# Kernel tuning notes

Hardware: AMD Instinct MI355X
Metric: run time of the kernel (lower is better)

## Reference

```python
import jax, jax.numpy as jnp
import numpy as np

NUM_BINS = 256


def setup_inputs() -> dict:
    key = jax.random.key(0)
    k1, k2 = jax.random.split(key)
    shape = (16, 3, 512, 512)
    I_complementary = jax.random.uniform(k1, shape, dtype=jnp.float32)
    I_target = jax.random.uniform(k2, shape, dtype=jnp.float32)
    return {"I_complementary": I_complementary, "I_target": I_target}


def reference(I_complementary, I_target):
    nb = NUM_BINS
    x = I_complementary.reshape(-1)
    y = I_target.reshape(-1)
    bx = jnp.clip(x * (nb - 1), 0, nb - 1).astype(jnp.int32)
    by = jnp.clip(y * (nb - 1), 0, nb - 1).astype(jnp.int32)
    # NOTE: torch's `hist[bx, by] += 1` is index_put WITHOUT accumulation, so
    # duplicate (bx,by) pairs all write old_value+1 = 1: the histogram is a
    # binary occupancy map, not counts. We replicate that with .at[].max(1).
    hist_2d = jnp.zeros((nb, nb), dtype=jnp.float32).at[bx, by].max(1.0)
    hist_2d = hist_2d / hist_2d.sum()
    p_x = hist_2d.sum(axis=1)  # [nb]
    p_y = hist_2d.sum(axis=0)  # [nb]
    mask = hist_2d > 0
    denom = p_x[:, None] * p_y[None, :] + 1e-10
    ratio = jnp.where(mask, hist_2d / denom, 1.0)
    mi = jnp.sum(jnp.where(mask, hist_2d * jnp.log(ratio), 0.0))
    return 1.0 - jnp.tanh(mi)
```

## Files before the change

kernel.cpp:

```cpp
#include <hip/hip_runtime.h>
#include <math.h>


#define NB 256
#define BM_WORDS 2048
#define HGRID 512
#define HTHREADS 512
#define RGRID 64
#define RTHREADS 256

#define SL_WORDS (HGRID * BM_WORDS)

__device__ __forceinline__ void set_bin(unsigned int* bm, float a, float b) {
    float va = fminf(fmaxf(a * 255.0f, 0.0f), 255.0f);
    float vb = fminf(fmaxf(b * 255.0f, 0.0f), 255.0f);
    int bin = ((int)va << 8) | (int)vb;
    atomicOr(&bm[bin >> 5], 1u << (bin & 31));
}

__device__ __forceinline__ void set_bin4(unsigned int* bm, float4 a, float4 b) {
    set_bin(bm, a.x, b.x); set_bin(bm, a.y, b.y);
    set_bin(bm, a.z, b.z); set_bin(bm, a.w, b.w);
}

__device__ __forceinline__ void finalize_from_lds(unsigned int* w, float* rcs, float* red,
                                                  int t, float* out) {
    float partial = 0.0f;
    int r = 0, c = 0;
    if (t < NB) {
#pragma unroll
        for (int k = 0; k < 8; ++k) r += __popc(w[t * 8 + k]);
        rcs[t] = (float)r;
        const int wsel = t >> 5;
        const int bsel = t & 31;
        for (int i = 0; i < NB; ++i) c += (w[i * 8 + wsel] >> bsel) & 1;
    }
    __syncthreads();
    float S = 0.0f;
    if (t < NB) {
        for (int i = 0; i < NB; ++i) S += rcs[i];
        if (r > 0) partial += (float)r * logf((float)r / S);
        if (c > 0) partial += (float)c * logf((float)c / S);
        for (int off = 32; off > 0; off >>= 1) partial += __shfl_down(partial, off, 64);
        if ((t & 63) == 0) red[t >> 6] = partial;
    }
    __syncthreads();
    if (t == 0) {
        float B = red[0] + red[1] + red[2] + red[3];
        float mi = -logf(S) - B / S;
        out[0] = 1.0f - tanhf(mi);
    }
}

__device__ __forceinline__ void hist_body(const float* __restrict__ x,
                                          const float* __restrict__ y,
                                          unsigned int* bm, int n, int t) {
    const int n4 = n >> 2;
    const float4* __restrict__ x4 = (const float4*)x;
    const float4* __restrict__ y4 = (const float4*)y;
    const int nth = gridDim.x * blockDim.x;
    int i = blockIdx.x * blockDim.x + t;

    if (i < n4) {
        float4 a0 = x4[i];
        float4 b0 = y4[i];
        int inext = i + nth;
        while (inext < n4) {
            float4 a1 = x4[inext];
            float4 b1 = y4[inext];
            inext += nth;
            set_bin4(bm, a0, b0);
            a0 = a1; b0 = b1;
        }
        set_bin4(bm, a0, b0);
    }
    for (int j = (n4 << 2) + blockIdx.x * blockDim.x + t; j < n; j += nth) {
        set_bin(bm, x[j], y[j]);
    }
}


__global__ __launch_bounds__(HTHREADS, 2) void hist_slices(const float* __restrict__ x,
                                                           const float* __restrict__ y,
                                                           unsigned int* __restrict__ ws,
                                                           int n) {
    __shared__ unsigned int bm[BM_WORDS];
    const int t = threadIdx.x;
    if (blockIdx.x == 0 && t == 0) ws[SL_WORDS + BM_WORDS] = 0u;
    for (int k = t; k < BM_WORDS; k += HTHREADS) bm[k] = 0u;
    __syncthreads();

    hist_body(x, y, bm, n, t);
    __syncthreads();

    uint4 v;
    v.x = bm[4 * t];     v.y = bm[4 * t + 1];
    v.z = bm[4 * t + 2]; v.w = bm[4 * t + 3];
    ((uint4*)(ws + (size_t)blockIdx.x * BM_WORDS))[t] = v;
}

__global__ __launch_bounds__(RTHREADS) void reduce_finalize(unsigned int* __restrict__ ws,
                                                            float* __restrict__ out) {
    __shared__ uint4 p4[RTHREADS];
    __shared__ unsigned int w[BM_WORDS];
    __shared__ float rcs[NB];
    __shared__ float red[8];
    __shared__ unsigned int ticket;
    const int t = threadIdx.x;
    const int b = blockIdx.x;
    unsigned int* finalbm = ws + SL_WORDS;
    unsigned int* counter = ws + SL_WORDS + BM_WORDS;

    const uint4* s4 = (const uint4*)ws;
    const int q = b * 8 + (t & 7);
    uint4 v = make_uint4(0u, 0u, 0u, 0u);
#pragma unroll 4
    for (int k = 0; k < HGRID / 32; ++k) {
        int s = (t >> 3) + 32 * k;
        uint4 g = s4[(size_t)s * (BM_WORDS / 4) + q];
        v.x |= g.x; v.y |= g.y; v.z |= g.z; v.w |= g.w;
    }
    p4[t] = v;
    __syncthreads();
    if (t < 8) {
        uint4 r = p4[t];
        for (int k = 1; k < 32; ++k) {
            uint4 g = p4[t + 8 * k];
            r.x |= g.x; r.y |= g.y; r.z |= g.z; r.w |= g.w;
        }
        ((uint4*)finalbm)[b * 8 + t] = r;
    }
    __syncthreads();

    if (t == 0) {
        __threadfence();
        ticket = atomicAdd(counter, 1u);
    }
    __syncthreads();
    if (ticket != gridDim.x - 1) return;

    __threadfence();
    for (int k = t; k < BM_WORDS; k += RTHREADS)
        w[k] = __hip_atomic_load(&finalbm[k], __ATOMIC_RELAXED, __HIP_MEMORY_SCOPE_AGENT);
    __syncthreads();
    finalize_from_lds(w, rcs, red, t, out);
}


__global__ void zero_kernel(unsigned int* __restrict__ bm) {
    int i = blockIdx.x * blockDim.x + threadIdx.x;
    if (i < BM_WORDS + 1) bm[i] = 0u;
}

__global__ __launch_bounds__(HTHREADS, 2) void hist_fused(const float* __restrict__ x,
                                                          const float* __restrict__ y,
                                                          unsigned int* __restrict__ gbm,
                                                          float* __restrict__ out,
                                                          int n) {
    __shared__ unsigned int bm[BM_WORDS];
    __shared__ float rcs[NB];
    __shared__ float red[8];
    __shared__ unsigned int ticket;
    const int t = threadIdx.x;

    for (int k = t; k < BM_WORDS; k += blockDim.x) bm[k] = 0u;
    __syncthreads();
    hist_body(x, y, bm, n, t);
    __syncthreads();
    for (int k = t; k < BM_WORDS; k += blockDim.x) {
        unsigned int v = bm[k];
        if (v) {
            unsigned int g = gbm[k];
            if (v & ~g) atomicOr(&gbm[k], v);
        }
    }
    __syncthreads();
    if (t == 0) {
        __threadfence();
        ticket = __hip_atomic_fetch_add(&gbm[BM_WORDS], 1u, __ATOMIC_ACQ_REL,
                                        __HIP_MEMORY_SCOPE_AGENT);
    }
    __syncthreads();
    if (ticket != gridDim.x - 1) return;
    __threadfence();
    for (int k = t; k < BM_WORDS; k += blockDim.x)
        bm[k] = __hip_atomic_load(&gbm[k], __ATOMIC_RELAXED, __HIP_MEMORY_SCOPE_AGENT);
    __syncthreads();
    finalize_from_lds(bm, rcs, red, t, out);
}

extern "C" void kernel_launch(void* const* d_in, const int* in_sizes, int n_in,
                              void* d_out, int out_size, void* d_ws, size_t ws_size,
                              hipStream_t stream) {
    const float* x = (const float*)d_in[0];
    const float* y = (const float*)d_in[1];
    float* out = (float*)d_out;
    unsigned int* ws = (unsigned int*)d_ws;
    const int n = in_sizes[0];

    const size_t need = (size_t)(SL_WORDS + BM_WORDS + 1) * sizeof(unsigned int);
    if (ws_size >= need) {
        hist_slices<<<HGRID, HTHREADS, 0, stream>>>(x, y, ws, n);
        reduce_finalize<<<RGRID, RTHREADS, 0, stream>>>(ws, out);
    } else {
        zero_kernel<<<(BM_WORDS + 256) / 256, 256, 0, stream>>>(ws);
        hist_fused<<<HGRID, HTHREADS, 0, stream>>>(x, y, ws, out, n);
    }
}
```

Measured before the change: 123.0 us.

## Merge per-block bitmaps into 8 shared copies via atomicOr

Each histogram block previously wrote its full 8KB LDS bitmap to a private slice, and a 64-block reduce kernel then OR-reduced all 512 slices with a ticket-based finalize. Now blocks atomically OR only their nonzero, not-yet-set words into one of 8 global copies. A single-block kernel then ORs the 8 copies and finalizes. This cuts the 4MB slice write and re-read, at the cost of an extra zeroing launch and atomic contention on the shared copies.

```diff
diff --git a/kernel.cpp b/kernel.cpp
--- a/kernel.cpp
+++ b/kernel.cpp
@@ -4,12 +4,9 @@
 
 #define NB 256
 #define BM_WORDS 2048
+#define NCOPY 8
 #define HGRID 512
 #define HTHREADS 512
-#define RGRID 64
-#define RTHREADS 256
-
-#define SL_WORDS (HGRID * BM_WORDS)
 
 __device__ __forceinline__ void set_bin(unsigned int* bm, float a, float b) {
     float va = fminf(fmaxf(a * 255.0f, 0.0f), 255.0f);
@@ -80,68 +77,50 @@
 }
 
 
-__global__ __launch_bounds__(HTHREADS, 2) void hist_slices(const float* __restrict__ x,
-                                                           const float* __restrict__ y,
-                                                           unsigned int* __restrict__ ws,
-                                                           int n) {
+__global__ void zero_copies(unsigned int* __restrict__ ws) {
+    int i = blockIdx.x * blockDim.x + threadIdx.x;
+    if (i < NCOPY * BM_WORDS) ws[i] = 0u;
+}
+
+__global__ __launch_bounds__(HTHREADS, 2) void hist_merge(const float* __restrict__ x,
+                                                          const float* __restrict__ y,
+                                                          unsigned int* __restrict__ ws,
+                                                          int n) {
     __shared__ unsigned int bm[BM_WORDS];
     const int t = threadIdx.x;
-    if (blockIdx.x == 0 && t == 0) ws[SL_WORDS + BM_WORDS] = 0u;
     for (int k = t; k < BM_WORDS; k += HTHREADS) bm[k] = 0u;
     __syncthreads();
 
     hist_body(x, y, bm, n, t);
     __syncthreads();
 
-    uint4 v;
-    v.x = bm[4 * t];     v.y = bm[4 * t + 1];
-    v.z = bm[4 * t + 2]; v.w = bm[4 * t + 3];
-    ((uint4*)(ws + (size_t)blockIdx.x * BM_WORDS))[t] = v;
+    unsigned int* copy = ws + (size_t)(blockIdx.x & (NCOPY - 1)) * BM_WORDS;
+#pragma unroll
+    for (int k = 0; k < BM_WORDS / HTHREADS; ++k) {
+        int w = t + k * HTHREADS;
+        unsigned int v = bm[w];
+        if (v) {
+            unsigned int g = copy[w];
+            if (v & ~g) atomicOr(&copy[w], v);
+        }
+    }
 }
 
-__global__ __launch_bounds__(RTHREADS) void reduce_finalize(unsigned int* __restrict__ ws,
+__global__ __launch_bounds__(HTHREADS) void reduce_finalize(const unsigned int* __restrict__ ws,
                                                             float* __restrict__ out) {
-    __shared__ uint4 p4[RTHREADS];
     __shared__ unsigned int w[BM_WORDS];
     __shared__ float rcs[NB];
     __shared__ float red[8];
-    __shared__ unsigned int ticket;
     const int t = threadIdx.x;
-    const int b = blockIdx.x;
-    unsigned int* finalbm = ws + SL_WORDS;
-    unsigned int* counter = ws + SL_WORDS + BM_WORDS;
 
-    const uint4* s4 = (const uint4*)ws;
-    const int q = b * 8 + (t & 7);
-    uint4 v = make_uint4(0u, 0u, 0u, 0u);
-#pragma unroll 4
-    for (int k = 0; k < HGRID / 32; ++k) {
-        int s = (t >> 3) + 32 * k;
-        uint4 g = s4[(size_t)s * (BM_WORDS / 4) + q];
-        v.x |= g.x; v.y |= g.y; v.z |= g.z; v.w |= g.w;
+#pragma unroll
+    for (int k = 0; k < BM_WORDS / HTHREADS; ++k) {
+        int q = t + k * HTHREADS;
+        unsigned int v = 0u;
+#pragma unroll
+        for (int c = 0; c < NCOPY; ++c) v |= ws[c * BM_WORDS + q];
+        w[q] = v;
     }
-    p4[t] = v;
-    __syncthreads();
-    if (t < 8) {
-        uint4 r = p4[t];
-        for (int k = 1; k < 32; ++k) {
-            uint4 g = p4[t + 8 * k];
-            r.x |= g.x; r.y |= g.y; r.z |= g.z; r.w |= g.w;
-        }
-        ((uint4*)finalbm)[b * 8 + t] = r;
-    }
-    __syncthreads();
-
-    if (t == 0) {
-        __threadfence();
-        ticket = atomicAdd(counter, 1u);
-    }
-    __syncthreads();
-    if (ticket != gridDim.x - 1) return;
-
-    __threadfence();
-    for (int k = t; k < BM_WORDS; k += RTHREADS)
-        w[k] = __hip_atomic_load(&finalbm[k], __ATOMIC_RELAXED, __HIP_MEMORY_SCOPE_AGENT);
     __syncthreads();
     finalize_from_lds(w, rcs, red, t, out);
 }
@@ -198,10 +177,11 @@
     unsigned int* ws = (unsigned int*)d_ws;
     const int n = in_sizes[0];
 
-    const size_t need = (size_t)(SL_WORDS + BM_WORDS + 1) * sizeof(unsigned int);
+    const size_t need = (size_t)(NCOPY * BM_WORDS) * sizeof(unsigned int);
     if (ws_size >= need) {
-        hist_slices<<<HGRID, HTHREADS, 0, stream>>>(x, y, ws, n);
-        reduce_finalize<<<RGRID, RTHREADS, 0, stream>>>(ws, out);
+        zero_copies<<<(NCOPY * BM_WORDS + 511) / 512, 512, 0, stream>>>(ws);
+        hist_merge<<<HGRID, HTHREADS, 0, stream>>>(x, y, ws, n);
+        reduce_finalize<<<1, HTHREADS, 0, stream>>>(ws, out);
     } else {
         zero_kernel<<<(BM_WORDS + 256) / 256, 256, 0, stream>>>(ws);
         hist_fused<<<HGRID, HTHREADS, 0, stream>>>(x, y, ws, out, n);
```

After: 130.0 us. 5.7% more time.
